# Performance work log

Hardware: AMD Instinct MI355X
Metric: run time of the kernel (lower is better)

## Reference

```python
import jax, jax.numpy as jnp
import numpy as np

B, S, H, NH, HD = 2, 2048, 1024, 16, 64
THETA = 10000.0


def setup_inputs() -> dict:
    key = jax.random.key(0)
    k1, k2, k3, k4, k5 = jax.random.split(key, 5)
    hidden_states = jax.random.normal(k1, (B, S, H), dtype=jnp.float32)
    # RoPE tables, interleaved-pair layout: [c0,c0,c1,c1,...] along head_dim
    inv_freq = 1.0 / (THETA ** (jnp.arange(0, HD, 2, dtype=jnp.float32) / HD))
    t = jnp.arange(S, dtype=jnp.float32)
    freqs = jnp.outer(t, inv_freq)                      # [S, HD//2]
    freqs_cos = jnp.repeat(jnp.cos(freqs), 2, axis=-1)  # [S, HD]
    freqs_sin = jnp.repeat(jnp.sin(freqs), 2, axis=-1)  # [S, HD]
    position_ids = jnp.arange(S, dtype=jnp.int32)
    w = 0.02
    Wq = jax.random.normal(k2, (H, H), dtype=jnp.float32) * w
    Wk = jax.random.normal(k3, (H, H), dtype=jnp.float32) * w
    Wv = jax.random.normal(k4, (H, H), dtype=jnp.float32) * w
    Wo = jax.random.normal(k5, (H, H), dtype=jnp.float32) * w
    return {"hidden_states": hidden_states, "freqs_cos": freqs_cos,
            "freqs_sin": freqs_sin, "position_ids": position_ids,
            "Wq": Wq, "Wk": Wk, "Wv": Wv, "Wo": Wo}


def _rotate_half_interleaved(x):
    # stack([-x[..., 1::2], x[..., ::2]], -1).reshape_as(x)
    xe = x.reshape(x.shape[:-1] + (HD // 2, 2))
    return jnp.stack([-xe[..., 1], xe[..., 0]], axis=-1).reshape(x.shape)


def reference(hidden_states, freqs_cos, freqs_sin, position_ids, Wq, Wk, Wv, Wo):
    b, s, _ = hidden_states.shape
    # QKV projections (torch Linear: y = x @ W.T), split into heads [b, nh, s, hd]
    q = jnp.einsum('bsh,oh->bso', hidden_states, Wq).reshape(b, s, NH, HD).transpose(0, 2, 1, 3)
    k = jnp.einsum('bsh,oh->bso', hidden_states, Wk).reshape(b, s, NH, HD).transpose(0, 2, 1, 3)
    v = jnp.einsum('bsh,oh->bso', hidden_states, Wv).reshape(b, s, NH, HD).transpose(0, 2, 1, 3)
    cos = freqs_cos[position_ids][None, None]  # [1, 1, s, hd]
    sin = freqs_sin[position_ids][None, None]
    rq = _rotate_half_interleaved(q)
    # NOTE: faithful to source bug — rotate_half_k is built from q, not k
    q = q * cos + rq * sin
    k = k * cos + rq * sin
    # causal SDPA, scale = 1/sqrt(head_dim)
    scores = jnp.einsum('bhqd,bhkd->bhqk', q, k) / jnp.sqrt(jnp.float32(HD))
    causal = jnp.tril(jnp.ones((s, s), dtype=bool))
    scores = jnp.where(causal, scores, jnp.float32(-1e30))
    attn = jax.nn.softmax(scores, axis=-1)
    out = jnp.einsum('bhqk,bhkd->bhqd', attn, v)
    out = out.transpose(0, 2, 1, 3).reshape(b, s, H)
    return jnp.einsum('bsh,oh->bso', out, Wo)
```

## Files before the change

### kernel.cpp

```cpp
#include <hip/hip_runtime.h>
#include <stdint.h>

#define BB 2
#define SS 2048
#define HH 1024
#define NHH 16
#define HDD 64

typedef short bf16s;
typedef __attribute__((ext_vector_type(8))) short short8;
typedef __attribute__((ext_vector_type(4))) short short4v;
typedef __attribute__((ext_vector_type(2))) short short2v;
typedef __attribute__((ext_vector_type(4))) float f32x4;
typedef _Float16 half4v __attribute__((ext_vector_type(4)));
typedef _Float16 half8v __attribute__((ext_vector_type(8)));
typedef __fp16 fp16x2 __attribute__((ext_vector_type(2)));

__device__ inline short f2bf(float f) {
  union { float f; uint32_t u; } v; v.f = f;
  uint32_t r = (v.u + 0x7fffu + ((v.u >> 16) & 1u)) >> 16;
  return (short)r;
}
__device__ inline float bf2f(short h) {
  union { uint32_t u; float f; } v; v.u = ((uint32_t)(uint16_t)h) << 16;
  return v.f;
}

__device__ inline void gld_lds16(const void* g, void* l) {
  __builtin_amdgcn_global_load_lds((const __attribute__((address_space(1))) void*)g,
                                   (__attribute__((address_space(3))) void*)l, 16, 0, 0);
}

__device__ inline void stv(short* C, size_t i, float v) { C[i] = f2bf(v); }
__device__ inline void stv(float* C, size_t i, float v) { C[i] = v; }

__global__ __launch_bounds__(256) void convert_all(
    const float* __restrict__ x, const float* __restrict__ Wq,
    const float* __restrict__ Wk, const float* __restrict__ Wv,
    const float* __restrict__ Wo, bf16s* __restrict__ xb,
    bf16s* __restrict__ wqkv, bf16s* __restrict__ wob) {
  const long M1 = 1024L * 1024L;
  long e = (long)(blockIdx.x * blockDim.x + threadIdx.x) * 4;
  const float* src; bf16s* dst;
  if (e < 4 * M1)      { src = x  + e;            dst = xb   + e; }
  else if (e < 5 * M1) { src = Wq + (e - 4 * M1); dst = wqkv + (e - 4 * M1); }
  else if (e < 6 * M1) { src = Wk + (e - 5 * M1); dst = wqkv + (e - 4 * M1); }
  else if (e < 7 * M1) { src = Wv + (e - 6 * M1); dst = wqkv + (e - 4 * M1); }
  else                 { src = Wo + (e - 7 * M1); dst = wob  + (e - 7 * M1); }
  float4 v = *(const float4*)src;
  short4v o;
  o.x = f2bf(v.x); o.y = f2bf(v.y); o.z = f2bf(v.z); o.w = f2bf(v.w);
  *(short4v*)dst = o;
}

template <typename OT>
__global__ __launch_bounds__(256) void gemm_bt(
    const bf16s* __restrict__ A, const bf16s* __restrict__ Bm,
    OT* __restrict__ C, int K, int ldc) {
  __shared__ __align__(16) bf16s As[128 * 64];
  __shared__ __align__(16) bf16s Bs[128 * 64];
  const int tid = threadIdx.x;
  const int lane = tid & 63, w = tid >> 6;
  const int quad = lane >> 4, mcol = lane & 15;
  const int bm = blockIdx.y * 128, bn = blockIdx.x * 128;
  const int wm = (w >> 1) * 64, wn = (w & 1) * 64;
  f32x4 acc[4][4] = {};
  const int nkt = K >> 6;
  for (int kt = 0; kt < nkt; ++kt) {
    __syncthreads();
#pragma unroll
    for (int i = 0; i < 4; ++i) {
      int seg = (i * 4 + w) * 512;
      int flat = seg + lane * 8;
      int row = flat >> 6;
      int cpos = (flat >> 3) & 7;
      int cs = cpos ^ (row & 7);
      gld_lds16(A + (size_t)(bm + row) * K + kt * 64 + cs * 8, &As[seg]);
      gld_lds16(Bm + (size_t)(bn + row) * K + kt * 64 + cs * 8, &Bs[seg]);
    }
    __syncthreads();
#pragma unroll
    for (int ks = 0; ks < 2; ++ks) {
      short8 af[4], bf[4];
#pragma unroll
      for (int mt = 0; mt < 4; ++mt) {
        int row = wm + mt * 16 + mcol;
        int cs = (ks * 4 + quad) ^ (row & 7);
        af[mt] = *(const short8*)&As[row * 64 + cs * 8];
      }
#pragma unroll
      for (int nt = 0; nt < 4; ++nt) {
        int row = wn + nt * 16 + mcol;
        int cs = (ks * 4 + quad) ^ (row & 7);
        bf[nt] = *(const short8*)&Bs[row * 64 + cs * 8];
      }
#pragma unroll
      for (int mt = 0; mt < 4; ++mt)
#pragma unroll
        for (int nt = 0; nt < 4; ++nt)
          acc[mt][nt] = __builtin_amdgcn_mfma_f32_16x16x32_bf16(af[mt], bf[nt], acc[mt][nt], 0, 0, 0);
    }
  }
#pragma unroll
  for (int mt = 0; mt < 4; ++mt)
#pragma unroll
    for (int nt = 0; nt < 4; ++nt) {
      int r0 = bm + wm + mt * 16 + quad * 4;
      int c = bn + wn + nt * 16 + mcol;
#pragma unroll
      for (int r = 0; r < 4; ++r)
        stv(C, (size_t)(r0 + r) * ldc + c, acc[mt][nt][r]);
    }
}

__global__ __launch_bounds__(256) void rope_qk(
    const bf16s* __restrict__ qkv, const float* __restrict__ fcos,
    const float* __restrict__ fsin, const int* __restrict__ pos,
    bf16s* __restrict__ Q, bf16s* __restrict__ Kc) {
  int t = blockIdx.x * blockDim.x + threadIdx.x;
  int i = t & 31;
  int h = (t >> 5) & 15;
  int m = t >> 9;
  int s = m & 2047, b = m >> 11;
  int p = pos[s];
  float c = fcos[p * 64 + 2 * i];
  float sn = fsin[p * 64 + 2 * i];
  const bf16s* qp = qkv + (size_t)m * 3072 + h * 64 + 2 * i;
  float q0 = bf2f(qp[0]), q1 = bf2f(qp[1]);
  float k0 = bf2f(qp[1024]), k1 = bf2f(qp[1025]);
  float rq0 = -q1, rq1 = q0;
  size_t o = ((size_t)(b * 16 + h) * 2048 + s) * 64 + 2 * i;
  short2v qo, ko;
  qo.x = f2bf(q0 * c + rq0 * sn); qo.y = f2bf(q1 * c + rq1 * sn);
  ko.x = f2bf(k0 * c + rq0 * sn); ko.y = f2bf(k1 * c + rq1 * sn);
  *(short2v*)&Q[o] = qo;
  *(short2v*)&Kc[o] = ko;
}

__global__ __launch_bounds__(256) void transpose_v(
    const bf16s* __restrict__ qkv, _Float16* __restrict__ Vt) {
  __shared__ __align__(16) _Float16 T[64 * 72];
  int st = blockIdx.x, bh = blockIdx.y;
  int b = bh >> 4, h = bh & 15;
  int tid = threadIdx.x;
  int m0 = b * 2048 + st * 64;
#pragma unroll
  for (int p2 = 0; p2 < 2; ++p2) {
    int sl = p2 * 32 + (tid >> 3);
    int ch = tid & 7;
    short8 v = *(const short8*)&qkv[(size_t)(m0 + sl) * 3072 + 2048 + h * 64 + ch * 8];
#pragma unroll
    for (int j = 0; j < 8; ++j) T[(ch * 8 + j) * 72 + sl] = (_Float16)bf2f(v[j]);
  }
  __syncthreads();
#pragma unroll
  for (int p2 = 0; p2 < 2; ++p2) {
    int dl = p2 * 32 + (tid >> 3);
    int ch = tid & 7;
    half8v v = *(const half8v*)&T[dl * 72 + ch * 8];
    *(half8v*)&Vt[((size_t)bh * 64 + dl) * 2048 + st * 64 + ch * 8] = v;
  }
}

__global__ __launch_bounds__(256) void attn(
    const bf16s* __restrict__ Q, const bf16s* __restrict__ Kb,
    const _Float16* __restrict__ Vt, bf16s* __restrict__ O) {
  __shared__ __align__(16) bf16s Ks[64 * 64];
  __shared__ __align__(16) _Float16 Vs[64 * 64];
  const int bh = blockIdx.y;
  const int tid = threadIdx.x, lane = tid & 63, w = tid >> 6;
  const int quad = lane >> 4, col = lane & 15;
  const size_t base = (size_t)bh * 2048 * 64;
  const _Float16* vbase = Vt + (size_t)bh * 64 * 2048;
  const int b = bh >> 4, h = bh & 15;

  for (int ti = 0; ti < 2; ++ti) {
    const int qb = ti ? (31 - (int)blockIdx.x) : (int)blockIdx.x;
    const int qrow = qb * 64 + w * 16 + col;
    short8 bq[2];
#pragma unroll
    for (int ks = 0; ks < 2; ++ks)
      bq[ks] = *(const short8*)&Q[base + (size_t)qrow * 64 + ks * 32 + quad * 8];
    f32x4 Oacc[4] = {};
    float m2 = -1e30f, l = 0.f;

    for (int kt = 0; kt <= qb; ++kt) {
      __syncthreads();
#pragma unroll
      for (int i = 0; i < 2; ++i) {
        int seg = (i * 4 + w) * 512;
        int flat = seg + lane * 8;
        int row = flat >> 6, cpos = (flat >> 3) & 7;
        int cs = cpos ^ (row & 7);
        gld_lds16(&Kb[base + (size_t)(kt * 64 + row) * 64 + cs * 8], &Ks[seg]);
        gld_lds16(&vbase[(size_t)row * 2048 + kt * 64 + cs * 8], &Vs[seg]);
      }
      __syncthreads();

      f32x4 sc[4];
#pragma unroll
      for (int t = 0; t < 4; ++t) {
        f32x4 s4 = {};
#pragma unroll
        for (int ks = 0; ks < 2; ++ks) {
          int krow = t * 16 + col;
          int cs = (ks * 4 + quad) ^ (krow & 7);
          short8 af = *(const short8*)&Ks[krow * 64 + cs * 8];
          s4 = __builtin_amdgcn_mfma_f32_16x16x32_bf16(af, bq[ks], s4, 0, 0, 0);
        }
        sc[t] = s4;
      }

      const bool diag = (kt == qb);
      float mloc = -1e30f;
#pragma unroll
      for (int t = 0; t < 4; ++t)
#pragma unroll
        for (int r = 0; r < 4; ++r) {
          float v = sc[t][r] * 0.125f;
          if (diag && (t * 16 + quad * 4 + r > w * 16 + col)) v = -1e30f;
          sc[t][r] = v;
          mloc = fmaxf(mloc, v);
        }
      mloc = fmaxf(mloc, __shfl_xor(mloc, 16));
      mloc = fmaxf(mloc, __shfl_xor(mloc, 32));
      float mnew = fmaxf(m2, mloc);
      float alpha = __expf(m2 - mnew);
      m2 = mnew;

      float ps = 0.f;
      half4v pa[4];
#pragma unroll
      for (int t = 0; t < 4; ++t) {
        float p0 = __expf(sc[t][0] - m2);
        float p1 = __expf(sc[t][1] - m2);
        float p2 = __expf(sc[t][2] - m2);
        float p3 = __expf(sc[t][3] - m2);
        ps += (p0 + p1) + (p2 + p3);
        union { fp16x2 h2[2]; half4v h4; } u;
        u.h2[0] = __builtin_amdgcn_cvt_pkrtz(p0, p1);
        u.h2[1] = __builtin_amdgcn_cvt_pkrtz(p2, p3);
        pa[t] = u.h4;
      }
      ps += __shfl_xor(ps, 16);
      ps += __shfl_xor(ps, 32);
      l = l * alpha + ps;

      float a4[4];
#pragma unroll
      for (int r = 0; r < 4; ++r) a4[r] = __shfl(alpha, quad * 4 + r);
#pragma unroll
      for (int dt = 0; dt < 4; ++dt)
#pragma unroll
        for (int r = 0; r < 4; ++r) Oacc[dt][r] *= a4[r];

#pragma unroll
      for (int t = 0; t < 4; ++t) {
#pragma unroll
        for (int dt = 0; dt < 4; ++dt) {
          int vrow = dt * 16 + col;
          int cp = (t * 2 + (quad >> 1)) ^ (vrow & 7);
          half4v bv = *(const half4v*)&Vs[vrow * 64 + cp * 8 + (quad & 1) * 4];
          Oacc[dt] = __builtin_amdgcn_mfma_f32_16x16x16f16(pa[t], bv, Oacc[dt], 0, 0, 0);
        }
      }
    }

    float l4[4];
#pragma unroll
    for (int r = 0; r < 4; ++r) l4[r] = __shfl(l, quad * 4 + r);
#pragma unroll
    for (int dt = 0; dt < 4; ++dt)
#pragma unroll
      for (int r = 0; r < 4; ++r) {
        int srow = qb * 64 + w * 16 + quad * 4 + r;
        O[((size_t)b * 2048 + srow) * 1024 + h * 64 + dt * 16 + col] =
            f2bf(Oacc[dt][r] / l4[r]);
      }
  }
}

extern "C" void kernel_launch(void* const* d_in, const int* in_sizes, int n_in,
                              void* d_out, int out_size, void* d_ws, size_t ws_size,
                              hipStream_t stream) {
  (void)in_sizes; (void)n_in; (void)out_size; (void)ws_size;
  const float* x  = (const float*)d_in[0];
  const float* fc = (const float*)d_in[1];
  const float* fs = (const float*)d_in[2];
  const int* pos  = (const int*)d_in[3];
  const float* Wq = (const float*)d_in[4];
  const float* Wk = (const float*)d_in[5];
  const float* Wv = (const float*)d_in[6];
  const float* Wo = (const float*)d_in[7];
  float* out = (float*)d_out;
  char* ws = (char*)d_ws;
  const size_t MB = 1024 * 1024;
  bf16s* xb   = (bf16s*)(ws);
  bf16s* wqkv = (bf16s*)(ws + 8 * MB);
  bf16s* wob  = (bf16s*)(ws + 14 * MB);
  bf16s* qkv  = (bf16s*)(ws + 16 * MB);
  bf16s* Qb   = (bf16s*)(ws + 40 * MB);
  bf16s* Kb   = (bf16s*)(ws + 48 * MB);
  _Float16* Vt = (_Float16*)(ws + 56 * MB);
  bf16s* Ob   = (bf16s*)(ws);

  convert_all<<<8192, 256, 0, stream>>>(x, Wq, Wk, Wv, Wo, xb, wqkv, wob);
  gemm_bt<bf16s><<<dim3(24, 32), 256, 0, stream>>>(xb, wqkv, qkv, 1024, 3072);
  rope_qk<<<8192, 256, 0, stream>>>(qkv, fc, fs, pos, Qb, Kb);
  transpose_v<<<dim3(32, 32), 256, 0, stream>>>(qkv, Vt);
  attn<<<dim3(16, 32), 256, 0, stream>>>(Qb, Kb, Vt, Ob);
  gemm_bt<float><<<dim3(8, 32), 256, 0, stream>>>(Ob, wob, out, 1024, 1024);
}
```

Measured before the change: 213.9 us.

## Process paired query blocks in one K/V sweep sharing loaded tiles

The attention kernel now handles both query blocks (x and 31-x) in a single pass over K/V tiles, reusing each loaded K and V tile for both blocks instead of reloading it in two separate loops. The softmax scale is folded into Q during RoPE and the exponentials switch to exp2 with a log2e multiply. V is staged through registers into a padded LDS layout rather than by a direct global-to-LDS copy, and the causal mask branch is taken only on diagonal tiles. This roughly halves K/V global traffic, at the cost of more registers for two accumulator sets and some imbalance across iterations.

```diff
diff --git a/kernel.cpp b/kernel.cpp
--- a/kernel.cpp
+++ b/kernel.cpp
@@ -131,8 +131,10 @@
   float rq0 = -q1, rq1 = q0;
   size_t o = ((size_t)(b * 16 + h) * 2048 + s) * 64 + 2 * i;
   short2v qo, ko;
-  qo.x = f2bf(q0 * c + rq0 * sn); qo.y = f2bf(q1 * c + rq1 * sn);
-  ko.x = f2bf(k0 * c + rq0 * sn); ko.y = f2bf(k1 * c + rq1 * sn);
+  qo.x = f2bf((q0 * c + rq0 * sn) * 0.125f);
+  qo.y = f2bf((q1 * c + rq1 * sn) * 0.125f);
+  ko.x = f2bf(k0 * c + rq0 * sn);
+  ko.y = f2bf(k1 * c + rq1 * sn);
   *(short2v*)&Q[o] = qo;
   *(short2v*)&Kc[o] = ko;
 }
@@ -162,110 +164,140 @@
   }
 }
 
+__device__ __forceinline__ void attn_step(
+    const bf16s* Ks, const _Float16* Vs, const short8* bq,
+    f32x4* Oacc, float& m2, float& l, bool diag,
+    int w, int quad, int col) {
+  f32x4 sc[4];
+#pragma unroll
+  for (int t = 0; t < 4; ++t) {
+    f32x4 s4 = {};
+#pragma unroll
+    for (int ks = 0; ks < 2; ++ks) {
+      int krow = t * 16 + col;
+      int cs = (ks * 4 + quad) ^ (krow & 7);
+      short8 af = *(const short8*)&Ks[krow * 64 + cs * 8];
+      s4 = __builtin_amdgcn_mfma_f32_16x16x32_bf16(af, bq[ks], s4, 0, 0, 0);
+    }
+    sc[t] = s4;
+  }
+  const float LOG2E = 1.4426950408889634f;
+  float mloc = -1e30f;
+  if (diag) {
+#pragma unroll
+    for (int t = 0; t < 4; ++t)
+#pragma unroll
+      for (int r = 0; r < 4; ++r) {
+        float v = sc[t][r] * LOG2E;
+        if (t * 16 + quad * 4 + r > w * 16 + col) v = -1e30f;
+        sc[t][r] = v;
+        mloc = fmaxf(mloc, v);
+      }
+  } else {
+#pragma unroll
+    for (int t = 0; t < 4; ++t)
+#pragma unroll
+      for (int r = 0; r < 4; ++r) {
+        float v = sc[t][r] * LOG2E;
+        sc[t][r] = v;
+        mloc = fmaxf(mloc, v);
+      }
+  }
+  mloc = fmaxf(mloc, __shfl_xor(mloc, 16));
+  mloc = fmaxf(mloc, __shfl_xor(mloc, 32));
+  float mnew = fmaxf(m2, mloc);
+  float alpha = exp2f(m2 - mnew);
+  m2 = mnew;
+
+  float ps = 0.f;
+  half4v pa[4];
+#pragma unroll
+  for (int t = 0; t < 4; ++t) {
+    float p0 = exp2f(sc[t][0] - m2);
+    float p1 = exp2f(sc[t][1] - m2);
+    float p2 = exp2f(sc[t][2] - m2);
+    float p3 = exp2f(sc[t][3] - m2);
+    ps += (p0 + p1) + (p2 + p3);
+    union { fp16x2 h2[2]; half4v h4; } u;
+    u.h2[0] = __builtin_amdgcn_cvt_pkrtz(p0, p1);
+    u.h2[1] = __builtin_amdgcn_cvt_pkrtz(p2, p3);
+    pa[t] = u.h4;
+  }
+  ps += __shfl_xor(ps, 16);
+  ps += __shfl_xor(ps, 32);
+  l = l * alpha + ps;
+
+  float a4[4];
+#pragma unroll
+  for (int r = 0; r < 4; ++r) a4[r] = __shfl(alpha, quad * 4 + r);
+#pragma unroll
+  for (int dt = 0; dt < 4; ++dt)
+#pragma unroll
+    for (int r = 0; r < 4; ++r) Oacc[dt][r] *= a4[r];
+
+#pragma unroll
+  for (int t = 0; t < 4; ++t) {
+#pragma unroll
+    for (int dt = 0; dt < 4; ++dt) {
+      int vrow = dt * 16 + col;
+      half4v bv = *(const half4v*)&Vs[vrow * 68 + t * 16 + quad * 4];
+      Oacc[dt] = __builtin_amdgcn_mfma_f32_16x16x16f16(pa[t], bv, Oacc[dt], 0, 0, 0);
+    }
+  }
+}
+
 __global__ __launch_bounds__(256) void attn(
     const bf16s* __restrict__ Q, const bf16s* __restrict__ Kb,
     const _Float16* __restrict__ Vt, bf16s* __restrict__ O) {
   __shared__ __align__(16) bf16s Ks[64 * 64];
-  __shared__ __align__(16) _Float16 Vs[64 * 64];
+  __shared__ __align__(16) _Float16 Vs[64 * 68];
   const int bh = blockIdx.y;
   const int tid = threadIdx.x, lane = tid & 63, w = tid >> 6;
   const int quad = lane >> 4, col = lane & 15;
   const size_t base = (size_t)bh * 2048 * 64;
   const _Float16* vbase = Vt + (size_t)bh * 64 * 2048;
   const int b = bh >> 4, h = bh & 15;
-
-  for (int ti = 0; ti < 2; ++ti) {
-    const int qb = ti ? (31 - (int)blockIdx.x) : (int)blockIdx.x;
-    const int qrow = qb * 64 + w * 16 + col;
-    short8 bq[2];
-#pragma unroll
-    for (int ks = 0; ks < 2; ++ks)
-      bq[ks] = *(const short8*)&Q[base + (size_t)qrow * 64 + ks * 32 + quad * 8];
-    f32x4 Oacc[4] = {};
-    float m2 = -1e30f, l = 0.f;
-
-    for (int kt = 0; kt <= qb; ++kt) {
-      __syncthreads();
-#pragma unroll
-      for (int i = 0; i < 2; ++i) {
-        int seg = (i * 4 + w) * 512;
-        int flat = seg + lane * 8;
-        int row = flat >> 6, cpos = (flat >> 3) & 7;
-        int cs = cpos ^ (row & 7);
-        gld_lds16(&Kb[base + (size_t)(kt * 64 + row) * 64 + cs * 8], &Ks[seg]);
-        gld_lds16(&vbase[(size_t)row * 2048 + kt * 64 + cs * 8], &Vs[seg]);
-      }
-      __syncthreads();
-
-      f32x4 sc[4];
-#pragma unroll
-      for (int t = 0; t < 4; ++t) {
-        f32x4 s4 = {};
-#pragma unroll
-        for (int ks = 0; ks < 2; ++ks) {
-          int krow = t * 16 + col;
-          int cs = (ks * 4 + quad) ^ (krow & 7);
-          short8 af = *(const short8*)&Ks[krow * 64 + cs * 8];
-          s4 = __builtin_amdgcn_mfma_f32_16x16x32_bf16(af, bq[ks], s4, 0, 0, 0);
-        }
-        sc[t] = s4;
-      }
-
-      const bool diag = (kt == qb);
-      float mloc = -1e30f;
-#pragma unroll
-      for (int t = 0; t < 4; ++t)
-#pragma unroll
-        for (int r = 0; r < 4; ++r) {
-          float v = sc[t][r] * 0.125f;
-          if (diag && (t * 16 + quad * 4 + r > w * 16 + col)) v = -1e30f;
-          sc[t][r] = v;
-          mloc = fmaxf(mloc, v);
-        }
-      mloc = fmaxf(mloc, __shfl_xor(mloc, 16));
-      mloc = fmaxf(mloc, __shfl_xor(mloc, 32));
-      float mnew = fmaxf(m2, mloc);
-      float alpha = __expf(m2 - mnew);
-      m2 = mnew;
-
-      float ps = 0.f;
-      half4v pa[4];
-#pragma unroll
-      for (int t = 0; t < 4; ++t) {
-        float p0 = __expf(sc[t][0] - m2);
-        float p1 = __expf(sc[t][1] - m2);
-        float p2 = __expf(sc[t][2] - m2);
-        float p3 = __expf(sc[t][3] - m2);
-        ps += (p0 + p1) + (p2 + p3);
-        union { fp16x2 h2[2]; half4v h4; } u;
-        u.h2[0] = __builtin_amdgcn_cvt_pkrtz(p0, p1);
-        u.h2[1] = __builtin_amdgcn_cvt_pkrtz(p2, p3);
-        pa[t] = u.h4;
-      }
-      ps += __shfl_xor(ps, 16);
-      ps += __shfl_xor(ps, 32);
-      l = l * alpha + ps;
-
-      float a4[4];
-#pragma unroll
-      for (int r = 0; r < 4; ++r) a4[r] = __shfl(alpha, quad * 4 + r);
-#pragma unroll
-      for (int dt = 0; dt < 4; ++dt)
-#pragma unroll
-        for (int r = 0; r < 4; ++r) Oacc[dt][r] *= a4[r];
-
-#pragma unroll
-      for (int t = 0; t < 4; ++t) {
-#pragma unroll
-        for (int dt = 0; dt < 4; ++dt) {
-          int vrow = dt * 16 + col;
-          int cp = (t * 2 + (quad >> 1)) ^ (vrow & 7);
-          half4v bv = *(const half4v*)&Vs[vrow * 64 + cp * 8 + (quad & 1) * 4];
-          Oacc[dt] = __builtin_amdgcn_mfma_f32_16x16x16f16(pa[t], bv, Oacc[dt], 0, 0, 0);
-        }
-      }
-    }
-
+  const int x = blockIdx.x;
+  const int qbA = 31 - x, qbB = x;
+
+  short8 bqA[2], bqB[2];
+  {
+    const int qrA = qbA * 64 + w * 16 + col;
+    const int qrB = qbB * 64 + w * 16 + col;
+#pragma unroll
+    for (int ks = 0; ks < 2; ++ks) {
+      bqA[ks] = *(const short8*)&Q[base + (size_t)qrA * 64 + ks * 32 + quad * 8];
+      bqB[ks] = *(const short8*)&Q[base + (size_t)qrB * 64 + ks * 32 + quad * 8];
+    }
+  }
+  f32x4 OA[4] = {}, OB[4] = {};
+  float mA = -1e30f, lA = 0.f, mB = -1e30f, lB = 0.f;
+
+  const int vd = tid >> 2, vc = tid & 3;
+  for (int kt = 0; kt <= qbA; ++kt) {
+    half8v vreg0 = *(const half8v*)&vbase[(size_t)vd * 2048 + kt * 64 + vc * 16];
+    half8v vreg1 = *(const half8v*)&vbase[(size_t)vd * 2048 + kt * 64 + vc * 16 + 8];
+    __syncthreads();
+    *(half8v*)&Vs[vd * 68 + vc * 16] = vreg0;
+    *(half8v*)&Vs[vd * 68 + vc * 16 + 8] = vreg1;
+#pragma unroll
+    for (int i = 0; i < 2; ++i) {
+      int seg = (i * 4 + w) * 512;
+      int flat = seg + lane * 8;
+      int row = flat >> 6, cpos = (flat >> 3) & 7;
+      int cs = cpos ^ (row & 7);
+      gld_lds16(&Kb[base + (size_t)(kt * 64 + row) * 64 + cs * 8], &Ks[seg]);
+    }
+    __syncthreads();
+    attn_step(Ks, Vs, bqA, OA, mA, lA, kt == qbA, w, quad, col);
+    if (kt <= qbB) attn_step(Ks, Vs, bqB, OB, mB, lB, kt == qbB, w, quad, col);
+  }
+
+#pragma unroll
+  for (int which = 0; which < 2; ++which) {
+    const int qb = which ? qbB : qbA;
+    const f32x4* Oacc = which ? OB : OA;
+    const float l = which ? lB : lA;
     float l4[4];
 #pragma unroll
     for (int r = 0; r < 4; ++r) l4[r] = __shfl(l, quad * 4 + r);
```

Result: faster. 209.5 us (-2.1%).
